# Kernel optimization log

Hardware: AMD Instinct MI355X
Metric: run time of the kernel (lower is better)

The kernel has to match this reference:

```python
import jax, jax.numpy as jnp
import numpy as np

D_MODEL = 1024
N_HEAD = 16
D_HEAD = 64
BSZ = 2
QLEN = 2048
LOCAL_SIZE = 1000
LN_EPS = 1e-5


def setup_inputs() -> dict:
    key = jax.random.key(0)
    ks = jax.random.split(key, 8)
    z1ss = jax.random.normal(ks[0], (BSZ, D_MODEL, QLEN), jnp.float32)
    pos_emb = jax.random.normal(ks[1], (1, D_MODEL, QLEN), jnp.float32)
    u1ss = jax.random.normal(ks[2], (BSZ, 3 * N_HEAD * D_HEAD, QLEN), jnp.float32) * 0.05
    W_qkv = jax.random.normal(ks[3], (3 * N_HEAD * D_HEAD, D_MODEL), jnp.float32) * 0.02
    W_r = jax.random.normal(ks[4], (N_HEAD * D_HEAD, D_MODEL), jnp.float32) * 0.02
    r_w_bias = jax.random.uniform(ks[5], (N_HEAD, D_HEAD), jnp.float32, -0.05, 0.05)
    r_r_bias = jax.random.uniform(ks[6], (N_HEAD, D_HEAD), jnp.float32, -0.05, 0.05)
    W_o = jax.random.normal(ks[7], (D_MODEL, N_HEAD * D_HEAD), jnp.float32) * 0.02
    b_o = jnp.zeros((D_MODEL,), jnp.float32)
    return dict(z1ss=z1ss, pos_emb=pos_emb, u1ss=u1ss, W_qkv=W_qkv, W_r=W_r,
                r_w_bias=r_w_bias, r_r_bias=r_r_bias, W_o=W_o, b_o=b_o)


def _rel_shift(x):
    # Transformer-XL relative-shift trick: pad one column on the left, reshape,
    # drop first row, reshape back. x: [b, n, qlen, klen]
    b, n, q, k = x.shape
    xp = jnp.pad(x, ((0, 0), (0, 0), (0, 0), (1, 0)))
    return xp.reshape(b, n, k + 1, q)[:, :, 1:, :].reshape(b, n, q, k)


def reference(z1ss, pos_emb, u1ss, W_qkv, W_r, r_w_bias, r_r_bias, W_o, b_o):
    bsz, d_model, qlen = z1ss.shape
    n_head, d_head = r_w_bias.shape
    klen = qlen  # mems=None -> mlen=0
    scale = 1.0 / (d_head ** 0.5)

    # Conv1d(kernel_size=1, bias=False) == per-position linear
    w_heads = jnp.einsum('od,bdq->boq', W_qkv, z1ss) + u1ss        # [b, 3*n*d, q]
    r_head_k = jnp.einsum('od,dq->oq', W_r, pos_emb[0]).reshape(n_head, d_head, klen)

    q_h, k_h, v_h = jnp.split(w_heads, 3, axis=1)
    q_h = q_h.reshape(bsz, n_head, d_head, qlen)
    k_h = k_h.reshape(bsz, n_head, d_head, klen)
    v_h = v_h.reshape(bsz, n_head, d_head, klen)

    AC = jnp.einsum('bndi,bndj->bnij', q_h + r_w_bias[:, :, None], k_h)
    BD = _rel_shift(jnp.einsum('bndi,ndj->bnij', q_h + r_r_bias[:, :, None], r_head_k))
    attn_score = (AC + BD) * scale                                  # [b, n, q, k]

    # causal + local-window mask (mlen=0)
    ones = jnp.ones((qlen, klen), dtype=bool)
    mask = jnp.triu(ones, 1) | jnp.tril(ones, -LOCAL_SIZE)
    attn_score = jnp.where(mask[None, None], -jnp.inf, attn_score)

    attn_prob = jax.nn.softmax(attn_score, axis=-1)
    attn_vec = jnp.einsum('bnij,bndj->bndi', attn_prob, v_h)
    attn_vec = attn_vec.reshape(bsz, n_head * d_head, qlen)

    attn_out = jnp.einsum('od,bdq->boq', W_o, attn_vec) + b_o[None, :, None]

    # post-LN residual: layer_norm over d_model (no affine params)
    x = (attn_out + z1ss).transpose(0, 2, 1)                        # [b, q, d]
    mu = x.mean(-1, keepdims=True)
    var = ((x - mu) ** 2).mean(-1, keepdims=True)
    x = (x - mu) / jnp.sqrt(var + LN_EPS)
    return x.transpose(0, 2, 1)                                     # [b, d, q]
```

## Files before the change

kernel.cpp:

```cpp
#include <hip/hip_runtime.h>
#include <hip/hip_bf16.h>

#define D_MODEL 1024
#define N_HEAD 16
#define BSZ 2
#define QLEN 2048
#define LOCAL_SIZE 1000
#define QKV3 (3 * N_HEAD * 64)

typedef __hip_bfloat16 bf16;
typedef short bf16x8 __attribute__((ext_vector_type(8)));
typedef float f32x4 __attribute__((ext_vector_type(4)));

static __device__ __forceinline__ float b2f(bf16 x) { return __bfloat162float(x); }
static __device__ __forceinline__ float bits2f(unsigned short u) {
    return __uint_as_float(((unsigned int)u) << 16);
}
static __device__ __forceinline__ unsigned short f2bs(float x) {
    __hip_bfloat16 h = __float2bfloat16(x);
    return *(unsigned short*)&h;
}

static __device__ __forceinline__ int rmode(int m, int fl) { return (m == 2) ? fl : m; }
static __device__ __forceinline__ float ldm(const void* p, size_t i, int isf) {
    return isf ? ((const float*)p)[i] : b2f(((const bf16*)p)[i]);
}
static __device__ __forceinline__ float4 ld4(const void* p, size_t i, int isf) {
    if (isf) return ((const float4*)p)[i >> 2];
    ushort4 u = ((const ushort4*)p)[i >> 2];
    float4 f;
    f.x = bits2f(u.x); f.y = bits2f(u.y); f.z = bits2f(u.z); f.w = bits2f(u.w);
    return f;
}
static __device__ __forceinline__ ushort4 cvt4(float4 f) {
    ushort4 u;
    u.x = f2bs(f.x); u.y = f2bs(f.y); u.z = f2bs(f.z); u.w = f2bs(f.w);
    return u;
}

static __device__ __forceinline__ void glds16(const bf16* g, unsigned short* l) {
    __builtin_amdgcn_global_load_lds(
        (const __attribute__((address_space(1))) void*)g,
        (__attribute__((address_space(3))) void*)l,
        16, 0, 0);
}

__global__ void detect_kernel(const unsigned short* __restrict__ w, int* __restrict__ flag)
{
    if (threadIdx.x == 0 && blockIdx.x == 0) {
        int good = 0;
        for (int i = 0; i < 256; ++i) {
            float v = bits2f(w[i]);
            if (v == v && fabsf(v) < 8.0f) ++good;
        }
        *flag = (good >= 240) ? 0 : 1;
    }
}

__global__ __launch_bounds__(256)
void convw(const void* __restrict__ in, bf16* __restrict__ out,
           const int* __restrict__ flag)
{
    const int fl = *flag;
    size_t i = ((size_t)blockIdx.x * 256 + threadIdx.x) * 8;
    if (fl) {
        float4 a = ((const float4*)in)[i / 4];
        float4 b = ((const float4*)in)[i / 4 + 1];
        *(ushort4*)((unsigned short*)out + i)     = cvt4(a);
        *(ushort4*)((unsigned short*)out + i + 4) = cvt4(b);
    } else {
        *(uint4*)((unsigned short*)out + i) = ((const uint4*)in)[i / 8];
    }
}

__global__ __launch_bounds__(256)
void transpose_cvt(const void* __restrict__ in, bf16* __restrict__ outp,
                   int rows, int cols, size_t sIn, size_t sOut,
                   const int* __restrict__ flag)
{
    const int fl = *flag;
    const int b  = blockIdx.z;
    const int c0 = blockIdx.x * 32;
    const int r0 = blockIdx.y * 32;
    const int tx = threadIdx.x & 31, ty = threadIdx.x >> 5;
    __shared__ float T[32][33];
#pragma unroll
    for (int r = 0; r < 4; ++r) {
        int rr = r0 + ty + r * 8;
        T[ty + r * 8][tx] = ldm(in, (size_t)b * sIn + (size_t)rr * cols + c0 + tx, fl);
    }
    __syncthreads();
#pragma unroll
    for (int r = 0; r < 4; ++r) {
        int cc = c0 + ty + r * 8;
        outp[(size_t)b * sOut + (size_t)cc * rows + r0 + tx] =
            __float2bfloat16(T[tx][ty + r * 8]);
    }
}

__global__ __launch_bounds__(256)
void gemm_glds(const bf16* __restrict__ A, size_t sAb,
               const bf16* __restrict__ B, size_t sBb,
               void* __restrict__ C, int c_is_bf16, size_t sCb,
               const void* __restrict__ addm, int mAdd, size_t sAddb,
               const void* __restrict__ bias, int mBias,
               int M, int N, int K, const int* __restrict__ flag)
{
    const int fl = *flag;
    const int fAdd = rmode(mAdd, fl), fBias = rmode(mBias, fl);

    const int bz = blockIdx.z;
    const int n0 = blockIdx.x * 128;
    const int m0 = blockIdx.y * 128;
    const int tid = threadIdx.x;
    const int wave = tid >> 6, lane = tid & 63;
    const int quad = lane >> 4, l15 = lane & 15;
    const int wm = (wave >> 1) * 64, wn = (wave & 1) * 64;

    __shared__ __align__(16) unsigned short A_s[2][128 * 32];
    __shared__ __align__(16) unsigned short B_s[2][128 * 32];

    const int srow = wave * 32 + (lane >> 2);
    const int scol = (lane & 3) * 8;
    const bf16* Ag = A + (size_t)bz * sAb + (size_t)(m0 + srow) * K + scol;
    const bf16* Bg = B + (size_t)bz * sBb + (size_t)(n0 + srow) * K + scol;
    const int sbase = wave * 1024;

    f32x4 acc[4][4];
#pragma unroll
    for (int i = 0; i < 4; ++i)
#pragma unroll
        for (int j = 0; j < 4; ++j) acc[i][j] = (f32x4){0.f, 0.f, 0.f, 0.f};

    glds16(Ag,                   &A_s[0][sbase]);
    glds16(Ag + (size_t)16 * K,  &A_s[0][sbase + 512]);
    glds16(Bg,                   &B_s[0][sbase]);
    glds16(Bg + (size_t)16 * K,  &B_s[0][sbase + 512]);

    int cur = 0;
    for (int k0 = 0; k0 < K; k0 += 32) {
        __syncthreads();
        if (k0 + 32 < K) {
            const int kn = k0 + 32;
            glds16(Ag + kn,                  &A_s[cur ^ 1][sbase]);
            glds16(Ag + (size_t)16 * K + kn, &A_s[cur ^ 1][sbase + 512]);
            glds16(Bg + kn,                  &B_s[cur ^ 1][sbase]);
            glds16(Bg + (size_t)16 * K + kn, &B_s[cur ^ 1][sbase + 512]);
        }
        bf16x8 a[4], bb[4];
#pragma unroll
        for (int i = 0; i < 4; ++i)
            a[i] = *(const bf16x8*)&A_s[cur][(wm + i * 16 + l15) * 32 + quad * 8];
#pragma unroll
        for (int j = 0; j < 4; ++j)
            bb[j] = *(const bf16x8*)&B_s[cur][(wn + j * 16 + l15) * 32 + quad * 8];
#pragma unroll
        for (int i = 0; i < 4; ++i)
#pragma unroll
            for (int j = 0; j < 4; ++j)
                acc[i][j] = __builtin_amdgcn_mfma_f32_16x16x32_bf16(a[i], bb[j], acc[i][j], 0, 0, 0);
        cur ^= 1;
    }

    const size_t cb = (size_t)bz * sCb;
#pragma unroll
    for (int i = 0; i < 4; ++i) {
#pragma unroll
        for (int j = 0; j < 4; ++j) {
            int n = n0 + wn + j * 16 + l15;
#pragma unroll
            for (int r = 0; r < 4; ++r) {
                int m = m0 + wm + i * 16 + quad * 4 + r;
                float v = acc[i][j][r];
                if (addm) v += ldm(addm, (size_t)bz * sAddb + (size_t)m * N + n, fAdd);
                if (bias) v += ldm(bias, (size_t)n, fBias);
                size_t ci = cb + (size_t)m * N + n;
                if (c_is_bf16) ((bf16*)C)[ci] = __float2bfloat16(v);
                else           ((float*)C)[ci] = v;
            }
        }
    }
}

__global__ __launch_bounds__(256)
void gemm_bf16(const void* __restrict__ A, int mA, size_t sAb,
               const void* __restrict__ B, int mB, size_t sBb,
               void* __restrict__ C, int c_is_bf16, size_t sCb,
               const void* __restrict__ addm, int mAdd, size_t sAddb,
               const void* __restrict__ bias, int mBias,
               int M, int N, int K, const int* __restrict__ flag)
{
    const int fl = *flag;
    const int fA = rmode(mA, fl), fB = rmode(mB, fl);
    const int fAdd = rmode(mAdd, fl), fBias = rmode(mBias, fl);

    const int bz = blockIdx.z;
    const int n0 = blockIdx.x * 128;
    const int m0 = blockIdx.y * 128;
    const int tid = threadIdx.x;
    const int wave = tid >> 6, lane = tid & 63;
    const int quad = lane >> 4, l15 = lane & 15;
    const int wm = (wave >> 1) * 64, wn = (wave & 1) * 64;

    __shared__ unsigned short A_s[128][40];
    __shared__ unsigned short B_s[128][40];

    const int r0c = tid >> 2,         c0c = tid & 3;
    const int r1c = (tid + 256) >> 2, c1c = tid & 3;

    const size_t aOff = (size_t)bz * sAb;
    const size_t bOff = (size_t)bz * sBb;
    const bf16*  Ah = (const bf16*)A;
    const float* Af = (const float*)A;
    const bf16*  Bh = (const bf16*)B;
    const float* Bf = (const float*)B;

    uint4 pa[4], pb[4];

#define LOAD_OP(p, fX, Xh, Xf, xOff, R0, C0, R1, C1, base, k0)                          \
    do {                                                                                \
        if (!fX) {                                                                      \
            p[0] = *(const uint4*)(Xh + xOff + (size_t)(base + R0) * K + (k0) + C0 * 8);\
            p[1] = *(const uint4*)(Xh + xOff + (size_t)(base + R1) * K + (k0) + C1 * 8);\
        } else {                                                                        \
            const float* q0 = Xf + xOff + (size_t)(base + R0) * K + (k0) + C0 * 8;      \
            const float* q1 = Xf + xOff + (size_t)(base + R1) * K + (k0) + C1 * 8;      \
            p[0] = *(const uint4*)q0; p[1] = *(const uint4*)(q0 + 4);                   \
            p[2] = *(const uint4*)q1; p[3] = *(const uint4*)(q1 + 4);                   \
        }                                                                               \
    } while (0)

#define WRITE_OP(p, fX, S, R0, C0, R1, C1)                                              \
    do {                                                                                \
        if (!fX) {                                                                      \
            *(uint4*)&S[R0][C0 * 8] = p[0];                                             \
            *(uint4*)&S[R1][C1 * 8] = p[1];                                             \
        } else {                                                                        \
            float4 f0 = *(float4*)&p[0], f1 = *(float4*)&p[1];                          \
            float4 f2 = *(float4*)&p[2], f3 = *(float4*)&p[3];                          \
            *(ushort4*)&S[R0][C0 * 8]     = cvt4(f0);                                   \
            *(ushort4*)&S[R0][C0 * 8 + 4] = cvt4(f1);                                   \
            *(ushort4*)&S[R1][C1 * 8]     = cvt4(f2);                                   \
            *(ushort4*)&S[R1][C1 * 8 + 4] = cvt4(f3);                                   \
        }                                                                               \
    } while (0)

    f32x4 acc[4][4];
#pragma unroll
    for (int i = 0; i < 4; ++i)
#pragma unroll
        for (int j = 0; j < 4; ++j) acc[i][j] = (f32x4){0.f, 0.f, 0.f, 0.f};

    LOAD_OP(pa, fA, Ah, Af, aOff, r0c, c0c, r1c, c1c, m0, 0);
    LOAD_OP(pb, fB, Bh, Bf, bOff, r0c, c0c, r1c, c1c, n0, 0);

    for (int k0 = 0; k0 < K; k0 += 32) {
        WRITE_OP(pa, fA, A_s, r0c, c0c, r1c, c1c);
        WRITE_OP(pb, fB, B_s, r0c, c0c, r1c, c1c);
        __syncthreads();

        const int kn = k0 + 32;
        if (kn < K) {
            LOAD_OP(pa, fA, Ah, Af, aOff, r0c, c0c, r1c, c1c, m0, kn);
            LOAD_OP(pb, fB, Bh, Bf, bOff, r0c, c0c, r1c, c1c, n0, kn);
        }

        bf16x8 a[4], bb[4];
#pragma unroll
        for (int i = 0; i < 4; ++i)
            a[i] = *(const bf16x8*)&A_s[wm + i * 16 + l15][quad * 8];
#pragma unroll
        for (int j = 0; j < 4; ++j)
            bb[j] = *(const bf16x8*)&B_s[wn + j * 16 + l15][quad * 8];
#pragma unroll
        for (int i = 0; i < 4; ++i)
#pragma unroll
            for (int j = 0; j < 4; ++j)
                acc[i][j] = __builtin_amdgcn_mfma_f32_16x16x32_bf16(a[i], bb[j], acc[i][j], 0, 0, 0);
        __syncthreads();
    }
#undef LOAD_OP
#undef WRITE_OP

    const size_t cb = (size_t)bz * sCb;
#pragma unroll
    for (int i = 0; i < 4; ++i) {
#pragma unroll
        for (int j = 0; j < 4; ++j) {
            int n = n0 + wn + j * 16 + l15;
#pragma unroll
            for (int r = 0; r < 4; ++r) {
                int m = m0 + wm + i * 16 + quad * 4 + r;
                float v = acc[i][j][r];
                if (addm) v += ldm(addm, (size_t)bz * sAddb + (size_t)m * N + n, fAdd);
                if (bias) v += ldm(bias, (size_t)n, fBias);
                size_t ci = cb + (size_t)m * N + n;
                if (c_is_bf16) ((bf16*)C)[ci] = __float2bfloat16(v);
                else           ((float*)C)[ci] = v;
            }
        }
    }
}

__global__ __launch_bounds__(256)
void gemm_tn(const void* __restrict__ A, int mA, size_t sAb,
             const void* __restrict__ Bsrc, int mB, int bTrans, int ldB, size_t sBb,
             void* __restrict__ C, int c_is_bf16, size_t sCb,
             const void* __restrict__ addm, int mAdd, int addT, size_t sAddb,
             const void* __restrict__ bias, int mBias,
             int M, int N, int K, const int* __restrict__ flag)
{
    const int fl = *flag;
    const int fA = rmode(mA, fl), fB = rmode(mB, fl);
    const int fAdd = rmode(mAdd, fl), fBias = rmode(mBias, fl);

    const int bz = blockIdx.z;
    const int n0 = blockIdx.x * 128;
    const int m0 = blockIdx.y * 128;
    const int tid = threadIdx.x;
    const int wave = tid >> 6, lane = tid & 63;
    const int quad = lane >> 4, l15 = lane & 15;
    const int wm = (wave >> 1) * 64, wn = (wave & 1) * 64;

    __shared__ unsigned short A_s[128][40];
    __shared__ unsigned short B_s[128][40];

    const size_t aBase = (size_t)bz * sAb;
    const size_t bBase = (size_t)bz * sBb;

    f32x4 acc[4][4];
#pragma unroll
    for (int i = 0; i < 4; ++i)
#pragma unroll
        for (int j = 0; j < 4; ++j) acc[i][j] = (f32x4){0.f, 0.f, 0.f, 0.f};

    for (int k0 = 0; k0 < K; k0 += 32) {
#pragma unroll
        for (int g = 0; g < 4; ++g) {
            int c = tid + g * 256;
            int m = c >> 3, kc = (c & 7) * 4;
            float4 f = ld4(A, aBase + (size_t)(m0 + m) * K + k0 + kc, fA);
            *(ushort4*)&A_s[m][kc] = cvt4(f);
        }
        if (!bTrans) {
#pragma unroll
            for (int g = 0; g < 4; ++g) {
                int c = tid + g * 256;
                int n = c >> 3, kc = (c & 7) * 4;
                float4 f = ld4(Bsrc, bBase + (size_t)(n0 + n) * ldB + k0 + kc, fB);
                *(ushort4*)&B_s[n][kc] = cvt4(f);
            }
        } else {
#pragma unroll
            for (int g = 0; g < 4; ++g) {
                int c = tid + g * 256;
                int k = c >> 5, nc = (c & 31) * 4;
                float4 f = ld4(Bsrc, bBase + (size_t)(k0 + k) * ldB + n0 + nc, fB);
                ushort4 u = cvt4(f);
                B_s[nc + 0][k] = u.x;
                B_s[nc + 1][k] = u.y;
                B_s[nc + 2][k] = u.z;
                B_s[nc + 3][k] = u.w;
            }
        }
        __syncthreads();

        bf16x8 a[4], bb[4];
#pragma unroll
        for (int i = 0; i < 4; ++i)
            a[i] = *(const bf16x8*)&A_s[wm + i * 16 + l15][quad * 8];
#pragma unroll
        for (int j = 0; j < 4; ++j)
            bb[j] = *(const bf16x8*)&B_s[wn + j * 16 + l15][quad * 8];
#pragma unroll
        for (int i = 0; i < 4; ++i)
#pragma unroll
            for (int j = 0; j < 4; ++j)
                acc[i][j] = __builtin_amdgcn_mfma_f32_16x16x32_bf16(a[i], bb[j], acc[i][j], 0, 0, 0);
        __syncthreads();
    }

    const size_t cb = (size_t)bz * sCb;
#pragma unroll
    for (int i = 0; i < 4; ++i) {
#pragma unroll
        for (int j = 0; j < 4; ++j) {
            int n = n0 + wn + j * 16 + l15;
#pragma unroll
            for (int r = 0; r < 4; ++r) {
                int m = m0 + wm + i * 16 + quad * 4 + r;
                float v = acc[i][j][r];
                if (addm) {
                    size_t ai = (size_t)bz * sAddb +
                                (addT ? ((size_t)n * M + m) : ((size_t)m * N + n));
                    v += ldm(addm, ai, fAdd);
                }
                if (bias) v += ldm(bias, (size_t)n, fBias);
                size_t ci = cb + (size_t)m * N + n;
                if (c_is_bf16) ((bf16*)C)[ci] = __float2bfloat16(v);
                else           ((float*)C)[ci] = v;
            }
        }
    }
}

__global__ __launch_bounds__(256)
void attn_mfma(const bf16* __restrict__ wh,
               const bf16* __restrict__ rhk,
               const void* __restrict__ rwb,
               const void* __restrict__ rrb,
               bf16* __restrict__ av_out,
               const int* __restrict__ flag)
{
    const int fl = *flag;
    const int it = blockIdx.x, h = blockIdx.y, b = blockIdx.z;
    const int i0 = it * 64;
    const int tid = threadIdx.x;
    const int wave = tid >> 6, lane = tid & 63;
    const int quad = lane >> 4, l15 = lane & 15;
    const int hw = h * 64;

    __shared__ __align__(16) unsigned short sm[18944];
    unsigned short* KtPs = sm;
    unsigned short* Vs   = sm + 4608;
    unsigned short* Rt   = sm + 9216;
    unsigned short* Gs   = sm + 9216;
    unsigned short* Qrw  = sm;
    unsigned short* Qrr  = sm + 4608;

    const bf16* whb = wh + (size_t)b * QKV3 * QLEN;
    const int d_t = tid & 63;
    const int dv0 = tid >> 3, jv0 = (tid & 7) * 8;
    const int dv1 = (tid + 256) >> 3;

    int lo = i0 - (LOCAL_SIZE - 1);
    if (lo < 0) lo = 0;
    const int jt_lo = lo >> 6;
    const int j0_lo = jt_lo * 64;

    {
        float brw = ldm(rwb, hw + d_t, fl);
        float brr = ldm(rrb, hw + d_t, fl);
        const bf16* qrow = whb + (size_t)(hw + d_t) * QLEN + i0;
        uint4 qv0 = *(const uint4*)(qrow + wave * 8);
        uint4 qv1 = *(const uint4*)(qrow + (4 + wave) * 8);
        const int pbase0 = j0_lo - i0 + QLEN - 64;
        const bf16* rrow = rhk + (size_t)(hw + d_t) * QLEN;
        uint4 rv0i = *(const uint4*)(rrow + pbase0 + wave * 8);
        uint4 rv1i = *(const uint4*)(rrow + pbase0 + (4 + wave) * 8);

        unsigned short u8[8];
        *(uint4*)u8 = qv0;
#pragma unroll
        for (int u = 0; u < 8; ++u) {
            float q = bits2f(u8[u]);
            Qrw[(wave * 8 + u) * 72 + d_t] = f2bs(q + brw);
            Qrr[(wave * 8 + u) * 72 + d_t] = f2bs(q + brr);
        }
        *(uint4*)u8 = qv1;
#pragma unroll
        for (int u = 0; u < 8; ++u) {
            float q = bits2f(u8[u]);
            Qrw[((4 + wave) * 8 + u) * 72 + d_t] = f2bs(q + brw);
            Qrr[((4 + wave) * 8 + u) * 72 + d_t] = f2bs(q + brr);
        }
        *(uint4*)u8 = rv0i;
#pragma unroll
        for (int u = 0; u < 8; ++u) Rt[(wave * 8 + u) * 72 + d_t] = u8[u];
        *(uint4*)u8 = rv1i;
#pragma unroll
        for (int u = 0; u < 8; ++u) Rt[((4 + wave) * 8 + u) * 72 + d_t] = u8[u];
    }

    uint4 kv0, kv1, vv0, vv1, rv0, rv1;
    {
        const int j0 = j0_lo;
        const bf16* krow = whb + (size_t)(1024 + hw + d_t) * QLEN + j0;
        kv0 = *(const uint4*)(krow + wave * 8);
        kv1 = *(const uint4*)(krow + (4 + wave) * 8);
        vv0 = *(const uint4*)(whb + (size_t)(2048 + hw + dv0) * QLEN + j0 + jv0);
        vv1 = *(const uint4*)(whb + (size_t)(2048 + hw + dv1) * QLEN + j0 + jv0);
        const int pn = j0 - i0 + QLEN;
        const bf16* rrow = rhk + (size_t)(hw + d_t) * QLEN;
        int p0 = pn + wave * 8;
        if (p0 + 7 < QLEN) rv0 = *(const uint4*)(rrow + p0);
        else {
            unsigned short u8[8];
#pragma unroll
            for (int u = 0; u < 8; ++u)
                u8[u] = (p0 + u < QLEN) ? *(const unsigned short*)(rrow + p0 + u) : 0;
            rv0 = *(uint4*)u8;
        }
        int p1 = pn + (4 + wave) * 8;
        if (p1 + 7 < QLEN) rv1 = *(const uint4*)(rrow + p1);
        else {
            unsigned short u8[8];
#pragma unroll
            for (int u = 0; u < 8; ++u)
                u8[u] = (p1 + u < QLEN) ? *(const unsigned short*)(rrow + p1 + u) : 0;
            rv1 = *(uint4*)u8;
        }
    }
    __syncthreads();

    const int qrow_off = (wave * 16 + l15) * 72 + quad * 8;
    bf16x8 qw0 = *(const bf16x8*)&Qrw[qrow_off];
    bf16x8 qw1 = *(const bf16x8*)&Qrw[qrow_off + 32];
    bf16x8 qr0 = *(const bf16x8*)&Qrr[qrow_off];
    bf16x8 qr1 = *(const bf16x8*)&Qrr[qrow_off + 32];

    f32x4 g_acc[8];
#pragma unroll
    for (int nt = 0; nt < 4; ++nt) {
        f32x4 g = (f32x4){0.f, 0.f, 0.f, 0.f};
        int ro = (nt * 16 + l15) * 72 + quad * 8;
        bf16x8 b0 = *(const bf16x8*)&Rt[ro];
        bf16x8 b1 = *(const bf16x8*)&Rt[ro + 32];
        g = __builtin_amdgcn_mfma_f32_16x16x32_bf16(qr0, b0, g, 0, 0, 0);
        g = __builtin_amdgcn_mfma_f32_16x16x32_bf16(qr1, b1, g, 0, 0, 0);
        g_acc[nt] = g;
    }

    float l_r[4] = {0.f, 0.f, 0.f, 0.f};
    f32x4 o_acc[4];
#pragma unroll
    for (int dj = 0; dj < 4; ++dj) o_acc[dj] = (f32x4){0.f, 0.f, 0.f, 0.f};

    for (int jt = jt_lo; jt <= it; ++jt) {
        const int j0 = jt * 64;
        __syncthreads();

        {
            unsigned short u8[8];
            *(uint4*)u8 = kv0;
#pragma unroll
            for (int u = 0; u < 8; ++u) KtPs[(wave * 8 + u) * 72 + d_t] = u8[u];
            *(uint4*)u8 = kv1;
#pragma unroll
            for (int u = 0; u < 8; ++u) KtPs[((4 + wave) * 8 + u) * 72 + d_t] = u8[u];
            *(uint4*)&Vs[dv0 * 72 + jv0] = vv0;
            *(uint4*)&Vs[dv1 * 72 + jv0] = vv1;
            *(uint4*)u8 = rv0;
#pragma unroll
            for (int u = 0; u < 8; ++u) Rt[(wave * 8 + u) * 72 + d_t] = u8[u];
            *(uint4*)u8 = rv1;
#pragma unroll
            for (int u = 0; u < 8; ++u) Rt[((4 + wave) * 8 + u) * 72 + d_t] = u8[u];
        }

        if (jt < it) {
            const int j0n = j0 + 64;
            const bf16* krow = whb + (size_t)(1024 + hw + d_t) * QLEN + j0n;
            kv0 = *(const uint4*)(krow + wave * 8);
            kv1 = *(const uint4*)(krow + (4 + wave) * 8);
            vv0 = *(const uint4*)(whb + (size_t)(2048 + hw + dv0) * QLEN + j0n + jv0);
            vv1 = *(const uint4*)(whb + (size_t)(2048 + hw + dv1) * QLEN + j0n + jv0);
            const int pn = j0n - i0 + QLEN;
            const bf16* rrow = rhk + (size_t)(hw + d_t) * QLEN;
            int p0 = pn + wave * 8;
            if (p0 + 7 < QLEN) rv0 = *(const uint4*)(rrow + p0);
            else {
                unsigned short u8[8];
#pragma unroll
                for (int u = 0; u < 8; ++u)
                    u8[u] = (p0 + u < QLEN) ? *(const unsigned short*)(rrow + p0 + u) : 0;
                rv0 = *(uint4*)u8;
            }
            int p1 = pn + (4 + wave) * 8;
            if (p1 + 7 < QLEN) rv1 = *(const uint4*)(rrow + p1);
            else {
                unsigned short u8[8];
#pragma unroll
                for (int u = 0; u < 8; ++u)
                    u8[u] = (p1 + u < QLEN) ? *(const unsigned short*)(rrow + p1 + u) : 0;
                rv1 = *(uint4*)u8;
            }
        }
        __syncthreads();

        f32x4 s_acc[4];
#pragma unroll
        for (int nj = 0; nj < 4; ++nj) {
            s_acc[nj] = (f32x4){0.f, 0.f, 0.f, 0.f};
            int ko = (nj * 16 + l15) * 72 + quad * 8;
            bf16x8 b0 = *(const bf16x8*)&KtPs[ko];
            bf16x8 b1 = *(const bf16x8*)&KtPs[ko + 32];
            s_acc[nj] = __builtin_amdgcn_mfma_f32_16x16x32_bf16(qw0, b0, s_acc[nj], 0, 0, 0);
            s_acc[nj] = __builtin_amdgcn_mfma_f32_16x16x32_bf16(qw1, b1, s_acc[nj], 0, 0, 0);
        }
#pragma unroll
        for (int nt = 0; nt < 4; ++nt) {
            f32x4 g = (f32x4){0.f, 0.f, 0.f, 0.f};
            int ro = (nt * 16 + l15) * 72 + quad * 8;
            bf16x8 b0 = *(const bf16x8*)&Rt[ro];
            bf16x8 b1 = *(const bf16x8*)&Rt[ro + 32];
            g = __builtin_amdgcn_mfma_f32_16x16x32_bf16(qr0, b0, g, 0, 0, 0);
            g = __builtin_amdgcn_mfma_f32_16x16x32_bf16(qr1, b1, g, 0, 0, 0);
            g_acc[4 + nt] = g;
        }
        __syncthreads();

#pragma unroll
        for (int nt = 0; nt < 8; ++nt) {
            ushort4 u;
            u.x = f2bs(g_acc[nt][0]);
            u.y = f2bs(g_acc[nt][1]);
            u.z = f2bs(g_acc[nt][2]);
            u.w = f2bs(g_acc[nt][3]);
            *(ushort4*)&Gs[(nt * 16 + l15) * 76 + wave * 16 + quad * 4] = u;
        }

        float rs[4] = {0.f, 0.f, 0.f, 0.f};
#pragma unroll
        for (int nj = 0; nj < 4; ++nj) {
#pragma unroll
            for (int r = 0; r < 4; ++r) {
                int i_loc = wave * 16 + quad * 4 + r;
                int j_loc = nj * 16 + l15;
                int t = j_loc - i_loc + 63;
                float bd = bits2f(Gs[t * 76 + i_loc]);
                int diff = (i0 + i_loc) - (j0 + j_loc);
                float p = 0.f;
                if (diff >= 0 && diff < LOCAL_SIZE)
                    p = __expf((s_acc[nj][r] + bd) * 0.125f);
                KtPs[i_loc * 72 + j_loc] = f2bs(p);
                rs[r] += p;
            }
        }
#pragma unroll
        for (int r = 0; r < 4; ++r) {
            float v = rs[r];
            v += __shfl_xor(v, 1);
            v += __shfl_xor(v, 2);
            v += __shfl_xor(v, 4);
            v += __shfl_xor(v, 8);
            l_r[r] += v;
        }

        {
            int po = (wave * 16 + l15) * 72 + quad * 8;
            bf16x8 pa0 = *(const bf16x8*)&KtPs[po];
            bf16x8 pa1 = *(const bf16x8*)&KtPs[po + 32];
#pragma unroll
            for (int dj = 0; dj < 4; ++dj) {
                int vo = (dj * 16 + l15) * 72 + quad * 8;
                bf16x8 b0 = *(const bf16x8*)&Vs[vo];
                bf16x8 b1 = *(const bf16x8*)&Vs[vo + 32];
                o_acc[dj] = __builtin_amdgcn_mfma_f32_16x16x32_bf16(pa0, b0, o_acc[dj], 0, 0, 0);
                o_acc[dj] = __builtin_amdgcn_mfma_f32_16x16x32_bf16(pa1, b1, o_acc[dj], 0, 0, 0);
            }
        }

#pragma unroll
        for (int nt = 0; nt < 4; ++nt) g_acc[nt] = g_acc[nt + 4];
    }

#pragma unroll
    for (int r = 0; r < 4; ++r) {
        float inv = 1.f / l_r[r];
        int q = i0 + wave * 16 + quad * 4 + r;
        bf16* orow = av_out + ((size_t)b * QLEN + q) * D_MODEL + hw;
#pragma unroll
        for (int dj = 0; dj < 4; ++dj)
            orow[dj * 16 + l15] = __float2bfloat16(o_acc[dj][r] * inv);
    }
}

__global__ __launch_bounds__(256)
void ln_kernel(float* __restrict__ yt)
{
    const int b = blockIdx.y, q = blockIdx.x;
    float* row = yt + ((size_t)b * QLEN + q) * D_MODEL;
    const int t = threadIdx.x;
    float4 v = ((float4*)row)[t];
    float s  = v.x + v.y + v.z + v.w;
    float ss = v.x * v.x + v.y * v.y + v.z * v.z + v.w * v.w;
#pragma unroll
    for (int off = 32; off; off >>= 1) {
        s  += __shfl_down(s, off);
        ss += __shfl_down(ss, off);
    }
    __shared__ float sw[4], ssw[4];
    const int w = t >> 6;
    if ((t & 63) == 0) { sw[w] = s; ssw[w] = ss; }
    __syncthreads();
    float S  = sw[0] + sw[1] + sw[2] + sw[3];
    float SS = ssw[0] + ssw[1] + ssw[2] + ssw[3];
    float mu  = S / D_MODEL;
    float var = SS / D_MODEL - mu * mu;
    float rs  = rsqrtf(var + 1e-5f);
    v.x = (v.x - mu) * rs; v.y = (v.y - mu) * rs;
    v.z = (v.z - mu) * rs; v.w = (v.w - mu) * rs;
    ((float4*)row)[t] = v;
}

__global__ __launch_bounds__(256)
void transpose_out(const float* __restrict__ yt, void* __restrict__ out,
                   const int* __restrict__ flag)
{
    const int fl = *flag;
    const int b  = blockIdx.z;
    const int q0 = blockIdx.x * 32;
    const int o0 = blockIdx.y * 32;
    const int tx = threadIdx.x & 31, ty = threadIdx.x >> 5;
    __shared__ float T[32][33];
#pragma unroll
    for (int r = 0; r < 4; ++r) {
        int q = q0 + ty + r * 8;
        T[ty + r * 8][tx] = yt[((size_t)b * QLEN + q) * D_MODEL + o0 + tx];
    }
    __syncthreads();
#pragma unroll
    for (int r = 0; r < 4; ++r) {
        int o = o0 + ty + r * 8;
        size_t oi = ((size_t)b * D_MODEL + o) * QLEN + q0 + tx;
        float v = T[tx][ty + r * 8];
        if (fl) ((float*)out)[oi] = v;
        else    ((bf16*)out)[oi] = __float2bfloat16(v);
    }
}

extern "C" void kernel_launch(void* const* d_in, const int* in_sizes, int n_in,
                              void* d_out, int out_size, void* d_ws, size_t ws_size,
                              hipStream_t stream)
{
    const void* z1ss = d_in[0];
    const void* pos  = d_in[1];
    const void* u1ss = d_in[2];
    const void* Wqkv = d_in[3];
    const void* Wr   = d_in[4];
    const void* rwb  = d_in[5];
    const void* rrb  = d_in[6];
    const void* Wo   = d_in[7];
    const void* bo   = d_in[8];

    const size_t whE  = (size_t)BSZ * QKV3 * QLEN;
    const size_t rhkE = (size_t)D_MODEL * QLEN;
    const size_t avE  = (size_t)BSZ * QLEN * D_MODEL;
    const size_t ztE  = avE;
    const size_t wqE  = (size_t)QKV3 * D_MODEL;
    const size_t wrE  = (size_t)D_MODEL * D_MODEL;
    const size_t woE  = wrE;

    char* ws = (char*)d_ws;
    bf16* wh   = (bf16*)ws;
    bf16* rhk  = wh + whE;
    bf16* avec = rhk + rhkE;
    bf16* post = avec;
    size_t baseB = (whE + rhkE + avE) * sizeof(bf16);
    bf16* zt  = (bf16*)(ws + baseB);
    bf16* wqb = zt + ztE;
    bf16* wrb = wqb + wqE;
    bf16* wob = wrb + wrE;
    float* yt = (float*)ws;

    const size_t t2B = baseB + ztE * sizeof(bf16) + 16;
    const size_t t1B = baseB + (ztE + wqE + wrE + woE) * sizeof(bf16) + 16;
    const int tier = (ws_size >= t1B) ? 1 : (ws_size >= t2B) ? 2 : 3;

    int* flag = (tier == 1) ? (int*)(wob + woE)
              : (tier == 2) ? (int*)(wqb)
                            : (int*)(ws + baseB);

    detect_kernel<<<1, 64, 0, stream>>>((const unsigned short*)Wqkv, flag);

    if (tier == 1) {
        convw<<<dim3(wqE / 2048), 256, 0, stream>>>(Wqkv, wqb, flag);
        convw<<<dim3(wrE / 2048), 256, 0, stream>>>(Wr,   wrb, flag);
        convw<<<dim3(woE / 2048), 256, 0, stream>>>(Wo,   wob, flag);

        transpose_cvt<<<dim3(QLEN / 32, D_MODEL / 32, BSZ), 256, 0, stream>>>(
            z1ss, zt, D_MODEL, QLEN, (size_t)D_MODEL * QLEN, (size_t)QLEN * D_MODEL, flag);
        transpose_cvt<<<dim3(QLEN / 32, D_MODEL / 32, 1), 256, 0, stream>>>(
            pos, post, D_MODEL, QLEN, 0, 0, flag);

        gemm_glds<<<dim3(2048 / 128, 3072 / 128, BSZ), 256, 0, stream>>>(
            wqb, 0,
            zt, (size_t)QLEN * D_MODEL,
            wh, 1, (size_t)QKV3 * QLEN,
            u1ss, 2, (size_t)QKV3 * QLEN,
            nullptr, 0,
            QKV3, QLEN, D_MODEL, flag);

        gemm_glds<<<dim3(2048 / 128, 1024 / 128, 1), 256, 0, stream>>>(
            wrb, 0,
            post, 0,
            rhk, 1, 0,
            nullptr, 0, 0,
            nullptr, 0,
            D_MODEL, QLEN, D_MODEL, flag);

        attn_mfma<<<dim3(QLEN / 64, N_HEAD, BSZ), 256, 0, stream>>>(
            wh, rhk, rwb, rrb, avec, flag);

        gemm_glds<<<dim3(1024 / 128, 2048 / 128, BSZ), 256, 0, stream>>>(
            avec, (size_t)QLEN * D_MODEL,
            wob, 0,
            yt, 0, (size_t)QLEN * D_MODEL,
            zt, 0, (size_t)QLEN * D_MODEL,
            bo, 2,
            QLEN, D_MODEL, D_MODEL, flag);
    } else if (tier == 2) {
        transpose_cvt<<<dim3(QLEN / 32, D_MODEL / 32, BSZ), 256, 0, stream>>>(
            z1ss, zt, D_MODEL, QLEN, (size_t)D_MODEL * QLEN, (size_t)QLEN * D_MODEL, flag);
        transpose_cvt<<<dim3(QLEN / 32, D_MODEL / 32, 1), 256, 0, stream>>>(
            pos, post, D_MODEL, QLEN, 0, 0, flag);

        gemm_bf16<<<dim3(2048 / 128, 3072 / 128, BSZ), 256, 0, stream>>>(
            Wqkv, 2, 0,
            zt, 0, (size_t)QLEN * D_MODEL,
            wh, 1, (size_t)QKV3 * QLEN,
            u1ss, 2, (size_t)QKV3 * QLEN,
            nullptr, 0,
            QKV3, QLEN, D_MODEL, flag);

        gemm_bf16<<<dim3(2048 / 128, 1024 / 128, 1), 256, 0, stream>>>(
            Wr, 2, 0,
            post, 0, 0,
            rhk, 1, 0,
            nullptr, 0, 0,
            nullptr, 0,
            D_MODEL, QLEN, D_MODEL, flag);

        attn_mfma<<<dim3(QLEN / 64, N_HEAD, BSZ), 256, 0, stream>>>(
            wh, rhk, rwb, rrb, avec, flag);

        gemm_bf16<<<dim3(1024 / 128, 2048 / 128, BSZ), 256, 0, stream>>>(
            avec, 0, (size_t)QLEN * D_MODEL,
            Wo, 2, 0,
            yt, 0, (size_t)QLEN * D_MODEL,
            zt, 0, (size_t)QLEN * D_MODEL,
            bo, 2,
            QLEN, D_MODEL, D_MODEL, flag);
    } else {
        gemm_tn<<<dim3(2048 / 128, 3072 / 128, BSZ), 256, 0, stream>>>(
            Wqkv, 2, 0,
            z1ss, 2, 1, QLEN, (size_t)D_MODEL * QLEN,
            wh, 1, (size_t)QKV3 * QLEN,
            u1ss, 2, 0, (size_t)QKV3 * QLEN,
            nullptr, 0,
            QKV3, QLEN, D_MODEL, flag);
        gemm_tn<<<dim3(2048 / 128, 1024 / 128, 1), 256, 0, stream>>>(
            Wr, 2, 0,
            pos, 2, 1, QLEN, 0,
            rhk, 1, 0,
            nullptr, 0, 0, 0,
            nullptr, 0,
            D_MODEL, QLEN, D_MODEL, flag);
        attn_mfma<<<dim3(QLEN / 64, N_HEAD, BSZ), 256, 0, stream>>>(
            wh, rhk, rwb, rrb, avec, flag);
        gemm_tn<<<dim3(1024 / 128, 2048 / 128, BSZ), 256, 0, stream>>>(
            avec, 0, (size_t)QLEN * D_MODEL,
            Wo, 2, 0, D_MODEL, 0,
            yt, 0, (size_t)QLEN * D_MODEL,
            z1ss, 2, 1, (size_t)D_MODEL * QLEN,
            bo, 2,
            QLEN, D_MODEL, D_MODEL, flag);
    }

    ln_kernel<<<dim3(QLEN, BSZ), 256, 0, stream>>>(yt);

    transpose_out<<<dim3(QLEN / 32, D_MODEL / 32, BSZ), 256, 0, stream>>>(yt, d_out, flag);
}
```

Baseline: 406.7 us.

## Split attention key range across two blocks and combine partial results

Each query tile's key-tile loop is split into two halves handled by separate blocks, which doubles the attention grid. This is meant to improve occupancy and reduce the load imbalance caused by the causal and local-window mask. Each block writes unnormalized fp32 output and row sums to a workspace. A new combine kernel adds the two halves and normalizes them into the bf16 attention vector. The cost is extra global traffic for the fp32 partials and one extra launch, and the path only runs when the workspace is large enough.

Result: slower. 423.5 us (+4.1%).

```diff
diff --git a/kernel.cpp b/kernel.cpp
--- a/kernel.cpp
+++ b/kernel.cpp
@@ -410,10 +410,15 @@
                const void* __restrict__ rwb,
                const void* __restrict__ rrb,
                bf16* __restrict__ av_out,
+               float* __restrict__ opart,
+               float* __restrict__ lpart,
                const int* __restrict__ flag)
 {
     const int fl = *flag;
-    const int it = blockIdx.x, h = blockIdx.y, b = blockIdx.z;
+    const int split = (opart != nullptr);
+    const int it   = split ? (blockIdx.x >> 1) : blockIdx.x;
+    const int half = split ? (blockIdx.x & 1) : 0;
+    const int h = blockIdx.y, b = blockIdx.z;
     const int i0 = it * 64;
     const int tid = threadIdx.x;
     const int wave = tid >> 6, lane = tid & 63;
@@ -436,7 +441,25 @@
     int lo = i0 - (LOCAL_SIZE - 1);
     if (lo < 0) lo = 0;
     const int jt_lo = lo >> 6;
-    const int j0_lo = jt_lo * 64;
+    const int nt = it - jt_lo + 1;
+    const int nA = (nt + 1) >> 1;
+    const int jt_s = split ? (half ? jt_lo + nA : jt_lo) : jt_lo;
+    const int jt_e = split ? (half ? it : jt_lo + nA - 1) : it;
+
+    if (split && jt_s > jt_e) {
+        float* obase = opart + ((size_t)half * BSZ + b) * QLEN * D_MODEL;
+        float* lbase = lpart + (((size_t)half * BSZ + b) * N_HEAD + h) * QLEN;
+#pragma unroll
+        for (int r = 0; r < 4; ++r) {
+            int q = i0 + wave * 16 + quad * 4 + r;
+            float* orow = obase + (size_t)q * D_MODEL + hw;
+#pragma unroll
+            for (int dj = 0; dj < 4; ++dj) orow[dj * 16 + l15] = 0.f;
+            if (l15 == 0) lbase[q] = 0.f;
+        }
+        return;
+    }
+    const int j0_s = jt_s * 64;
 
     {
         float brw = ldm(rwb, hw + d_t, fl);
@@ -444,7 +467,7 @@
         const bf16* qrow = whb + (size_t)(hw + d_t) * QLEN + i0;
         uint4 qv0 = *(const uint4*)(qrow + wave * 8);
         uint4 qv1 = *(const uint4*)(qrow + (4 + wave) * 8);
-        const int pbase0 = j0_lo - i0 + QLEN - 64;
+        const int pbase0 = j0_s - i0 + QLEN - 64;
         const bf16* rrow = rhk + (size_t)(hw + d_t) * QLEN;
         uint4 rv0i = *(const uint4*)(rrow + pbase0 + wave * 8);
         uint4 rv1i = *(const uint4*)(rrow + pbase0 + (4 + wave) * 8);
@@ -474,7 +497,7 @@
 
     uint4 kv0, kv1, vv0, vv1, rv0, rv1;
     {
-        const int j0 = j0_lo;
+        const int j0 = j0_s;
         const bf16* krow = whb + (size_t)(1024 + hw + d_t) * QLEN + j0;
         kv0 = *(const uint4*)(krow + wave * 8);
         kv1 = *(const uint4*)(krow + (4 + wave) * 8);
@@ -511,14 +534,14 @@
 
     f32x4 g_acc[8];
 #pragma unroll
-    for (int nt = 0; nt < 4; ++nt) {
+    for (int nt2 = 0; nt2 < 4; ++nt2) {
         f32x4 g = (f32x4){0.f, 0.f, 0.f, 0.f};
-        int ro = (nt * 16 + l15) * 72 + quad * 8;
+        int ro = (nt2 * 16 + l15) * 72 + quad * 8;
         bf16x8 b0 = *(const bf16x8*)&Rt[ro];
         bf16x8 b1 = *(const bf16x8*)&Rt[ro + 32];
         g = __builtin_amdgcn_mfma_f32_16x16x32_bf16(qr0, b0, g, 0, 0, 0);
         g = __builtin_amdgcn_mfma_f32_16x16x32_bf16(qr1, b1, g, 0, 0, 0);
-        g_acc[nt] = g;
+        g_acc[nt2] = g;
     }
 
     float l_r[4] = {0.f, 0.f, 0.f, 0.f};
@@ -526,7 +549,7 @@
 #pragma unroll
     for (int dj = 0; dj < 4; ++dj) o_acc[dj] = (f32x4){0.f, 0.f, 0.f, 0.f};
 
-    for (int jt = jt_lo; jt <= it; ++jt) {
+    for (int jt = jt_s; jt <= jt_e; ++jt) {
         const int j0 = jt * 64;
         __syncthreads();
 
@@ -548,7 +571,7 @@
             for (int u = 0; u < 8; ++u) Rt[((4 + wave) * 8 + u) * 72 + d_t] = u8[u];
         }
 
-        if (jt < it) {
+        if (jt < jt_e) {
             const int j0n = j0 + 64;
             const bf16* krow = whb + (size_t)(1024 + hw + d_t) * QLEN + j0n;
             kv0 = *(const uint4*)(krow + wave * 8);
@@ -589,25 +612,25 @@
             s_acc[nj] = __builtin_amdgcn_mfma_f32_16x16x32_bf16(qw1, b1, s_acc[nj], 0, 0, 0);
         }
 #pragma unroll
-        for (int nt = 0; nt < 4; ++nt) {
+        for (int nt2 = 0; nt2 < 4; ++nt2) {
             f32x4 g = (f32x4){0.f, 0.f, 0.f, 0.f};
-            int ro = (nt * 16 + l15) * 72 + quad * 8;
+            int ro = (nt2 * 16 + l15) * 72 + quad * 8;
             bf16x8 b0 = *(const bf16x8*)&Rt[ro];
             bf16x8 b1 = *(const bf16x8*)&Rt[ro + 32];
             g = __builtin_amdgcn_mfma_f32_16x16x32_bf16(qr0, b0, g, 0, 0, 0);
             g = __builtin_amdgcn_mfma_f32_16x16x32_bf16(qr1, b1, g, 0, 0, 0);
-            g_acc[4 + nt] = g;
+            g_acc[4 + nt2] = g;
         }
         __syncthreads();
 
 #pragma unroll
-        for (int nt = 0; nt < 8; ++nt) {
+        for (int nt2 = 0; nt2 < 8; ++nt2) {
             ushort4 u;
-            u.x = f2bs(g_acc[nt][0]);
-            u.y = f2bs(g_acc[nt][1]);
-            u.z = f2bs(g_acc[nt][2]);
-            u.w = f2bs(g_acc[nt][3]);
-            *(ushort4*)&Gs[(nt * 16 + l15) * 76 + wave * 16 + quad * 4] = u;
+            u.x = f2bs(g_acc[nt2][0]);
+            u.y = f2bs(g_acc[nt2][1]);
+            u.z = f2bs(g_acc[nt2][2]);
+            u.w = f2bs(g_acc[nt2][3]);
+            *(ushort4*)&Gs[(nt2 * 16 + l15) * 76 + wave * 16 + quad * 4] = u;
         }
 
         float rs[4] = {0.f, 0.f, 0.f, 0.f};
@@ -652,18 +675,56 @@
         }
 
 #pragma unroll
-        for (int nt = 0; nt < 4; ++nt) g_acc[nt] = g_acc[nt + 4];
-    }
-
-#pragma unroll
-    for (int r = 0; r < 4; ++r) {
-        float inv = 1.f / l_r[r];
-        int q = i0 + wave * 16 + quad * 4 + r;
-        bf16* orow = av_out + ((size_t)b * QLEN + q) * D_MODEL + hw;
-#pragma unroll
-        for (int dj = 0; dj < 4; ++dj)
-            orow[dj * 16 + l15] = __float2bfloat16(o_acc[dj][r] * inv);
-    }
+        for (int nt2 = 0; nt2 < 4; ++nt2) g_acc[nt2] = g_acc[nt2 + 4];
+    }
+
+    if (split) {
+        float* obase = opart + ((size_t)half * BSZ + b) * QLEN * D_MODEL;
+        float* lbase = lpart + (((size_t)half * BSZ + b) * N_HEAD + h) * QLEN;
+#pragma unroll
+        for (int r = 0; r < 4; ++r) {
+            int q = i0 + wave * 16 + quad * 4 + r;
+            float* orow = obase + (size_t)q * D_MODEL + hw;
+#pragma unroll
+            for (int dj = 0; dj < 4; ++dj)
+                orow[dj * 16 + l15] = o_acc[dj][r];
+            if (l15 == 0) lbase[q] = l_r[r];
+        }
+    } else {
+#pragma unroll
+        for (int r = 0; r < 4; ++r) {
+            float inv = 1.f / l_r[r];
+            int q = i0 + wave * 16 + quad * 4 + r;
+            bf16* orow = av_out + ((size_t)b * QLEN + q) * D_MODEL + hw;
+#pragma unroll
+            for (int dj = 0; dj < 4; ++dj)
+                orow[dj * 16 + l15] = __float2bfloat16(o_acc[dj][r] * inv);
+        }
+    }
+}
+
+__global__ __launch_bounds__(256)
+void combine_attn(const float* __restrict__ opart, const float* __restrict__ lpart,
+                  bf16* __restrict__ avec)
+{
+    size_t idx = ((size_t)blockIdx.x * 256 + threadIdx.x) * 4;
+    const int d = idx & (D_MODEL - 1);
+    const int q = (int)((idx >> 10) & (QLEN - 1));
+    const int b = (int)(idx >> 21);
+    const int h = d >> 6;
+    const size_t oHalf = (size_t)BSZ * QLEN * D_MODEL;
+    const size_t o_i = ((size_t)b * QLEN + q) * D_MODEL + d;
+    float4 o1 = *(const float4*)(opart + o_i);
+    float4 o2 = *(const float4*)(opart + oHalf + o_i);
+    const size_t lHalf = (size_t)BSZ * N_HEAD * QLEN;
+    const size_t l_i = ((size_t)b * N_HEAD + h) * QLEN + q;
+    float inv = 1.f / (lpart[l_i] + lpart[lHalf + l_i]);
+    float4 o;
+    o.x = (o1.x + o2.x) * inv;
+    o.y = (o1.y + o2.y) * inv;
+    o.z = (o1.z + o2.z) * inv;
+    o.w = (o1.w + o2.w) * inv;
+    *(ushort4*)((unsigned short*)avec + idx) = cvt4(o);
 }
 
 __global__ __launch_bounds__(256)
@@ -741,6 +802,8 @@
     const size_t wqE  = (size_t)QKV3 * D_MODEL;
     const size_t wrE  = (size_t)D_MODEL * D_MODEL;
     const size_t woE  = wrE;
+    const size_t opE  = (size_t)2 * BSZ * QLEN * D_MODEL;
+    const size_t lpE  = (size_t)2 * BSZ * N_HEAD * QLEN;
 
     char* ws = (char*)d_ws;
     bf16* wh   = (bf16*)ws;
@@ -752,19 +815,24 @@
     bf16* wqb = zt + ztE;
     bf16* wrb = wqb + wqE;
     bf16* wob = wrb + wrE;
+    float* opart = (float*)(wob + woE);
+    float* lpart = opart + opE;
     float* yt = (float*)ws;
 
     const size_t t2B = baseB + ztE * sizeof(bf16) + 16;
     const size_t t1B = baseB + (ztE + wqE + wrE + woE) * sizeof(bf16) + 16;
-    const int tier = (ws_size >= t1B) ? 1 : (ws_size >= t2B) ? 2 : 3;
-
-    int* flag = (tier == 1) ? (int*)(wob + woE)
+    const size_t t0B = t1B + (opE + lpE) * sizeof(float);
+    const int tier = (ws_size >= t0B) ? 0 : (ws_size >= t1B) ? 1
+                   : (ws_size >= t2B) ? 2 : 3;
+
+    int* flag = (tier == 0) ? (int*)(lpart + lpE)
+              : (tier == 1) ? (int*)(wob + woE)
               : (tier == 2) ? (int*)(wqb)
                             : (int*)(ws + baseB);
 
     detect_kernel<<<1, 64, 0, stream>>>((const unsigned short*)Wqkv, flag);
 
-    if (tier == 1) {
+    if (tier <= 1) {
         convw<<<dim3(wqE / 2048), 256, 0, stream>>>(Wqkv, wqb, flag);
         convw<<<dim3(wrE / 2048), 256, 0, stream>>>(Wr,   wrb, flag);
         convw<<<dim3(woE / 2048), 256, 0, stream>>>(Wo,   wob, flag);
@@ -790,8 +858,15 @@
             nullptr, 0,
             D_MODEL, QLEN, D_MODEL, flag);
 
-        attn_mfma<<<dim3(QLEN / 64, N_HEAD, BSZ), 256, 0, stream>>>(
-            wh, rhk, rwb, rrb, avec, flag);
+        if (tier == 0) {
+            attn_mfma<<<dim3(QLEN / 64 * 2, N_HEAD, BSZ), 256, 0, stream>>>(
+                wh, rhk, rwb, rrb, avec, opart, lpart, flag);
+            combine_attn<<<dim3((unsigned)(avE / 4 / 256)), 256, 0, stream>>>(
+                opart, lpart, avec);
+        } else {
+            attn_mfma<<<dim3(QLEN / 64, N_HEAD, BSZ), 256, 0, stream>>>(
+                wh, rhk, rwb, rrb, avec, nullptr, nullptr, flag);
+        }
 
         gemm_glds<<<dim3(1024 / 128, 2048 / 128, BSZ), 256, 0, stream>>>(
             avec, (size_t)QLEN * D_MODEL,
@@ -823,7 +898,7 @@
             D_MODEL, QLEN, D_MODEL, flag);
 
         attn_mfma<<<dim3(QLEN / 64, N_HEAD, BSZ), 256, 0, stream>>>(
-            wh, rhk, rwb, rrb, avec, flag);
+            wh, rhk, rwb, rrb, avec, nullptr, nullptr, flag);
 
         gemm_bf16<<<dim3(1024 / 128, 2048 / 128, BSZ), 256, 0, stream>>>(
             avec, 0, (size_t)QLEN * D_MODEL,
@@ -848,7 +923,7 @@
             nullptr, 0,
             D_MODEL, QLEN, D_MODEL, flag);
         attn_mfma<<<dim3(QLEN / 64, N_HEAD, BSZ), 256, 0, stream>>>(
-            wh, rhk, rwb, rrb, avec, flag);
+            wh, rhk, rwb, rrb, avec, nullptr, nullptr, flag);
         gemm_tn<<<dim3(1024 / 128, 2048 / 128, BSZ), 256, 0, stream>>>(
             avec, 0, (size_t)QLEN * D_MODEL,
             Wo, 2, 0, D_MODEL, 0,
```
